# Kernel optimization log

Hardware: AMD Instinct MI355X
Metric: run time of the kernel (lower is better)

## Reference

```python
import jax, jax.numpy as jnp
import numpy as np
import math

B, S, D, H = 2, 2048, 2048, 16
HD = D // H  # head_dim = 128


def _rope_tables(seq_len, head_dim, theta=10000.0):
    inv = 1.0 / (theta ** (np.arange(0, head_dim, 2, dtype=np.float32) / head_dim))
    t = np.arange(seq_len, dtype=np.float32)
    freqs = np.outer(t, inv)  # [S, HD/2]
    return jnp.asarray(np.cos(freqs)), jnp.asarray(np.sin(freqs))


def setup_inputs() -> dict:
    key = jax.random.key(0)
    ks = jax.random.split(key, 6)
    std = 1.0 / math.sqrt(D)
    x = jax.random.normal(ks[0], (B, S, D), dtype=jnp.float32)
    wq_w = jax.random.normal(ks[1], (D, D), dtype=jnp.float32) * std
    wk_w = jax.random.normal(ks[2], (D, D), dtype=jnp.float32) * std
    wv_w = jax.random.normal(ks[3], (D, D), dtype=jnp.float32) * std
    wo_w = jax.random.normal(ks[4], (D, D), dtype=jnp.float32) * std
    zb = jnp.zeros((D,), dtype=jnp.float32)
    fc, fs = _rope_tables(S, HD)
    return {"x": x, "wq_w": wq_w, "wq_b": zb, "wk_w": wk_w, "wk_b": zb,
            "wv_w": wv_w, "wv_b": zb, "wo_w": wo_w, "wo_b": zb,
            "freqs_cos": fc, "freqs_sin": fs}


def _apply_rope(q, k, cos, sin):
    # q, k: [B, S, H, HD]; cos/sin: [S, HD/2] -> broadcast [1, S, 1, HD/2]
    cos = cos[None, :, None, :]
    sin = sin[None, :, None, :]

    def rot(t):
        tr, ti = t[..., 0::2], t[..., 1::2]
        orr = tr * cos - ti * sin
        oi = tr * sin + ti * cos
        return jnp.stack([orr, oi], axis=-1).reshape(t.shape)

    return rot(q), rot(k)


def reference(x, wq_w, wq_b, wk_w, wk_b, wv_w, wv_b, wo_w, wo_b, freqs_cos, freqs_sin):
    b, s, d = x.shape
    q = (x @ wq_w.T + wq_b).reshape(b, s, H, HD)
    k = (x @ wk_w.T + wk_b).reshape(b, s, H, HD)
    v = (x @ wv_w.T + wv_b).reshape(b, s, H, HD)
    q, k = _apply_rope(q, k, freqs_cos[:s], freqs_sin[:s])
    q = q.transpose(0, 2, 1, 3)  # [B,H,S,HD]
    k = k.transpose(0, 2, 1, 3)
    v = v.transpose(0, 2, 1, 3)
    scale = math.sqrt(HD)
    scores = jnp.einsum('bhqd,bhkd->bhqk', q, k) / scale
    causal = jnp.tril(jnp.ones((s, s), dtype=bool))
    scores = jnp.where(causal[None, None], scores, jnp.float32(-jnp.inf))
    attn = jax.nn.softmax(scores, axis=-1)
    out = jnp.einsum('bhqk,bhkd->bhqd', attn, v)
    out = out.transpose(0, 2, 1, 3).reshape(b, s, d)
    out = out @ wo_w.T + wo_b
    return out, k, v
```

## Files before the change

### kernel.cpp

```cpp
#include <hip/hip_runtime.h>

#define B_  2
#define S_  2048
#define D_  2048
#define H_  16
#define HD_ 128

#define QSCALE 0.1275174319003887f

typedef __attribute__((ext_vector_type(4))) float  f32x4;
typedef __attribute__((ext_vector_type(8))) short  short8;
typedef __attribute__((ext_vector_type(8))) __bf16 bf16x8;
typedef __attribute__((ext_vector_type(4))) float  floatv4;
typedef __attribute__((ext_vector_type(4))) unsigned short ushortv4;

__device__ inline unsigned short f2bf(float f) {
  unsigned int u = __builtin_bit_cast(unsigned int, f);
  u += 0x7fffu + ((u >> 16) & 1u);
  return (unsigned short)(u >> 16);
}

__device__ inline void gld16(void* lds, const void* g) {
  __builtin_amdgcn_global_load_lds(
      (const __attribute__((address_space(1))) unsigned int*)g,
      (__attribute__((address_space(3))) unsigned int*)lds, 16, 0, 0);
}

__device__ inline bf16x8 lds_frag(const unsigned short* p) {
  return __builtin_bit_cast(bf16x8, *(const short8*)p);
}

__global__ void cvt_all(const float* __restrict__ x,
                        const float* __restrict__ w0, const float* __restrict__ w1,
                        const float* __restrict__ w2, const float* __restrict__ w3,
                        unsigned short* __restrict__ xb,
                        unsigned short* __restrict__ wb0, unsigned short* __restrict__ wb1,
                        unsigned short* __restrict__ wb2, unsigned short* __restrict__ wb3) {
  int i = blockIdx.x * 256 + threadIdx.x;
  const float* s; unsigned short* d; int off;
  if (i < 2097152) { s = x; d = xb; off = i; }
  else {
    int j = i - 2097152;
    int r = j >> 20; off = j & 1048575;
    s = (r == 0) ? w0 : (r == 1) ? w1 : (r == 2) ? w2 : w3;
    d = (r == 0) ? wb0 : (r == 1) ? wb1 : (r == 2) ? wb2 : wb3;
  }
  floatv4 v = ((const floatv4*)s)[off];
  ushortv4 o;
  o.x = f2bf(v.x); o.y = f2bf(v.y); o.z = f2bf(v.z); o.w = f2bf(v.w);
  ((ushortv4*)d)[off] = o;
}

__global__ __launch_bounds__(256, 2)
void gemm_nt(const unsigned short* __restrict__ A,
             const unsigned short* __restrict__ W,
             const float* __restrict__ bias,
             float* __restrict__ C, int M, int N, int K) {
  __shared__ __attribute__((aligned(16))) unsigned short As[128 * 32];
  __shared__ __attribute__((aligned(16))) unsigned short Bs[128 * 32];
  const int t = threadIdx.x;
  const int w = t >> 6, lane = t & 63;
  const int quad = lane >> 4, l16 = lane & 15;
  const int m0 = blockIdx.y * 128, n0 = blockIdx.x * 128;
  const int wm = (w >> 1) * 64, wn = (w & 1) * 64;
  f32x4 acc[4][4] = {};

  for (int k0 = 0; k0 < K; k0 += 32) {
    __syncthreads();
#pragma unroll
    for (int j = 0; j < 2; ++j) {
      int o = (t + 256 * j) * 16;
      int row = o >> 6, cb = o & 63;
      gld16((char*)As + w * 1024 + j * 4096,
            (const char*)(A + (size_t)(m0 + row) * K + k0) + cb);
      gld16((char*)Bs + w * 1024 + j * 4096,
            (const char*)(W + (size_t)(n0 + row) * K + k0) + cb);
    }
    __syncthreads();
    bf16x8 af[4], bfr[4];
#pragma unroll
    for (int i = 0; i < 4; ++i)
      af[i] = lds_frag(As + (wm + i * 16 + l16) * 32 + quad * 8);
#pragma unroll
    for (int j = 0; j < 4; ++j)
      bfr[j] = lds_frag(Bs + (wn + j * 16 + l16) * 32 + quad * 8);
#pragma unroll
    for (int i = 0; i < 4; ++i)
#pragma unroll
      for (int j = 0; j < 4; ++j)
        acc[i][j] = __builtin_amdgcn_mfma_f32_16x16x32_bf16(af[i], bfr[j], acc[i][j], 0, 0, 0);
  }

#pragma unroll
  for (int j = 0; j < 4; ++j) {
    int col = n0 + wn + j * 16 + l16;
    float bv = bias[col];
#pragma unroll
    for (int i = 0; i < 4; ++i)
#pragma unroll
      for (int r = 0; r < 4; ++r) {
        int row = m0 + wm + i * 16 + quad * 4 + r;
        C[(size_t)row * N + col] = acc[i][j][r] + bv;
      }
  }
}

__global__ void rope_kernel(const float* __restrict__ Qbuf,
                            const float* __restrict__ Kbuf,
                            const float* __restrict__ fc,
                            const float* __restrict__ fs,
                            unsigned short* __restrict__ Qa,
                            unsigned short* __restrict__ Ka,
                            float* __restrict__ k_out) {
  int idx = blockIdx.x * 256 + threadIdx.x;
  int i = idx & 63;
  int h = (idx >> 6) & (H_ - 1);
  int s = (idx >> 10) & (S_ - 1);
  int b = idx >> 21;
  size_t src = ((size_t)(b * S_ + s)) * D_ + h * HD_ + 2 * i;
  float2 q = *(const float2*)(Qbuf + src);
  float2 k = *(const float2*)(Kbuf + src);
  float c = fc[s * 64 + i], sn = fs[s * 64 + i];
  float qor = q.x * c - q.y * sn, qoi = q.x * sn + q.y * c;
  float kor = k.x * c - k.y * sn, koi = k.x * sn + k.y * c;
  size_t dst = ((size_t)((b * H_ + h) * S_ + s)) * HD_ + 2 * i;
  *(unsigned int*)(Qa + dst) = (unsigned int)f2bf(qor * QSCALE) | ((unsigned int)f2bf(qoi * QSCALE) << 16);
  *(unsigned int*)(Ka + dst) = (unsigned int)f2bf(kor) | ((unsigned int)f2bf(koi) << 16);
  *(float2*)(k_out + dst) = make_float2(kor, koi);
}

__global__ void vtrans_kernel(const float* __restrict__ Vbuf,
                              float* __restrict__ v_out,
                              unsigned short* __restrict__ Vt) {
  __shared__ float tile[64][33];
  int t = threadIdx.x;
  int s0 = blockIdx.x * 64, d0 = blockIdx.y * 32, bh = blockIdx.z;
  int b = bh >> 4, h = bh & 15;
#pragma unroll
  for (int rr = 0; rr < 8; ++rr) {
    int sl = rr * 8 + (t >> 5), dl = t & 31;
    float v = Vbuf[((size_t)(b * S_ + s0 + sl)) * D_ + h * HD_ + d0 + dl];
    tile[sl][dl] = v;
    v_out[((size_t)(bh * S_ + s0 + sl)) * HD_ + d0 + dl] = v;
  }
  __syncthreads();
#pragma unroll
  for (int rr = 0; rr < 8; ++rr) {
    int dl = rr * 4 + (t >> 6), sl = t & 63;
    Vt[((size_t)(bh * HD_ + d0 + dl)) * S_ + s0 + sl] = f2bf(tile[sl][dl]);
  }
}

__global__ __launch_bounds__(256, 2)
void attn_kernel(const unsigned short* __restrict__ Qa,
                 const unsigned short* __restrict__ Ka,
                 const unsigned short* __restrict__ Vt,
                 unsigned short* __restrict__ Oa) {
  __shared__ __attribute__((aligned(16))) unsigned short Ks[2][64 * 128];
  __shared__ __attribute__((aligned(16))) unsigned short Vs[128 * 64];
  __shared__ __attribute__((aligned(16))) unsigned short Ps[4][32 * 64];
  const int t = threadIdx.x, w = t >> 6, lane = t & 63;
  const int quad = lane >> 4, l16 = lane & 15;
  const int bh = blockIdx.y, b = bh >> 4, h = bh & 15;
  const unsigned short* Qp = Qa + (size_t)bh * S_ * HD_;
  const unsigned short* Kp = Ka + (size_t)bh * S_ * HD_;
  const unsigned short* Vp = Vt + (size_t)bh * HD_ * S_;
  const float NEGINF = -__builtin_inff();

  for (int part = 0; part < 2; ++part) {
    const int qt = part ? (15 - (int)blockIdx.x) : (int)blockIdx.x;
    const int q0 = qt * 128;
    const int ntmax = 2 * qt + 1;

    __syncthreads();

#pragma unroll
    for (int j = 0; j < 4; ++j) {
      int o = (t + 256 * j) * 16;
      int row = o >> 8, cb = o & 255;
      gld16((char*)Ks[0] + w * 1024 + j * 4096, (const char*)(Kp + (size_t)row * HD_) + cb);
    }
    bf16x8 qf[2][4];
#pragma unroll
    for (int mi = 0; mi < 2; ++mi)
#pragma unroll
      for (int kk = 0; kk < 4; ++kk)
        qf[mi][kk] = *(const bf16x8*)(Qp + (size_t)(q0 + w * 32 + mi * 16 + l16) * HD_ + kk * 32 + quad * 8);

    float m_i[2][4], l_i[2][4];
#pragma unroll
    for (int mi = 0; mi < 2; ++mi)
#pragma unroll
      for (int r = 0; r < 4; ++r) { m_i[mi][r] = NEGINF; l_i[mi][r] = 0.f; }
    f32x4 oacc[2][8] = {};
    int c = 0;

    for (int nt = 0; nt <= ntmax; ++nt) {
      __syncthreads();

#pragma unroll
      for (int j = 0; j < 4; ++j) {
        int o = (t + 256 * j) * 16;
        int vrow = o >> 7, vcb = o & 127;
        gld16((char*)Vs + w * 1024 + j * 4096,
              (const char*)(Vp + (size_t)vrow * S_ + nt * 64) + vcb);
      }

      f32x4 sacc[2][4] = {};
      const unsigned short* Kc = Ks[c];
#pragma unroll
      for (int j = 0; j < 4; ++j)
#pragma unroll
        for (int kk = 0; kk < 4; ++kk) {
          bf16x8 kf = lds_frag(Kc + (j * 16 + l16) * 128 + kk * 32 + quad * 8);
          sacc[0][j] = __builtin_amdgcn_mfma_f32_16x16x32_bf16(qf[0][kk], kf, sacc[0][j], 0, 0, 0);
          sacc[1][j] = __builtin_amdgcn_mfma_f32_16x16x32_bf16(qf[1][kk], kf, sacc[1][j], 0, 0, 0);
        }

      const bool dotail = (nt >= 2 * qt);
      float rowmax[2][4], alpha[2][4], rowsum[2][4];
#pragma unroll
      for (int mi = 0; mi < 2; ++mi)
#pragma unroll
        for (int r = 0; r < 4; ++r) rowmax[mi][r] = NEGINF;
#pragma unroll
      for (int mi = 0; mi < 2; ++mi)
#pragma unroll
        for (int j = 0; j < 4; ++j) {
          int scol = nt * 64 + j * 16 + l16;
#pragma unroll
          for (int r = 0; r < 4; ++r) {
            float v = sacc[mi][j][r];
            if (dotail && scol > q0 + w * 32 + mi * 16 + quad * 4 + r) v = NEGINF;
            sacc[mi][j][r] = v;
            rowmax[mi][r] = fmaxf(rowmax[mi][r], v);
          }
        }
#pragma unroll
      for (int off = 1; off < 16; off <<= 1)
#pragma unroll
        for (int mi = 0; mi < 2; ++mi)
#pragma unroll
          for (int r = 0; r < 4; ++r)
            rowmax[mi][r] = fmaxf(rowmax[mi][r], __shfl_xor(rowmax[mi][r], off));
#pragma unroll
      for (int mi = 0; mi < 2; ++mi)
#pragma unroll
        for (int r = 0; r < 4; ++r) {
          float mnew = fmaxf(m_i[mi][r], rowmax[mi][r]);
          alpha[mi][r] = __builtin_amdgcn_exp2f(m_i[mi][r] - mnew);
          m_i[mi][r] = mnew;
          rowsum[mi][r] = 0.f;
        }
#pragma unroll
      for (int mi = 0; mi < 2; ++mi)
#pragma unroll
        for (int j = 0; j < 4; ++j)
#pragma unroll
          for (int r = 0; r < 4; ++r) {
            float e = __builtin_amdgcn_exp2f(sacc[mi][j][r] - m_i[mi][r]);
            sacc[mi][j][r] = e;
            rowsum[mi][r] += e;
          }
#pragma unroll
      for (int off = 1; off < 16; off <<= 1)
#pragma unroll
        for (int mi = 0; mi < 2; ++mi)
#pragma unroll
          for (int r = 0; r < 4; ++r)
            rowsum[mi][r] += __shfl_xor(rowsum[mi][r], off);
#pragma unroll
      for (int mi = 0; mi < 2; ++mi)
#pragma unroll
        for (int r = 0; r < 4; ++r) l_i[mi][r] = l_i[mi][r] * alpha[mi][r] + rowsum[mi][r];
#pragma unroll
      for (int mi = 0; mi < 2; ++mi)
#pragma unroll
        for (int f = 0; f < 8; ++f)
#pragma unroll
          for (int r = 0; r < 4; ++r) oacc[mi][f][r] *= alpha[mi][r];

      __syncthreads();

      if (nt < ntmax) {
#pragma unroll
        for (int j = 0; j < 4; ++j) {
          int o = (t + 256 * j) * 16;
          int row = o >> 8, cb = o & 255;
          gld16((char*)Ks[c ^ 1] + w * 1024 + j * 4096,
                (const char*)(Kp + (size_t)((nt + 1) * 64 + row) * HD_) + cb);
        }
      }

      unsigned short* Pw = &Ps[w][0];
#pragma unroll
      for (int mi = 0; mi < 2; ++mi)
#pragma unroll
        for (int j = 0; j < 4; ++j)
#pragma unroll
          for (int r = 0; r < 4; ++r)
            Pw[(mi * 16 + quad * 4 + r) * 64 + j * 16 + l16] = f2bf(sacc[mi][j][r]);
      asm volatile("s_waitcnt lgkmcnt(0)" ::: "memory");

#pragma unroll
      for (int s2 = 0; s2 < 2; ++s2) {
        bf16x8 pf0 = lds_frag(Pw + (l16) * 64 + s2 * 32 + quad * 8);
        bf16x8 pf1 = lds_frag(Pw + (16 + l16) * 64 + s2 * 32 + quad * 8);
#pragma unroll
        for (int f = 0; f < 8; ++f) {
          bf16x8 vf = lds_frag(Vs + (f * 16 + l16) * 64 + s2 * 32 + quad * 8);
          oacc[0][f] = __builtin_amdgcn_mfma_f32_16x16x32_bf16(pf0, vf, oacc[0][f], 0, 0, 0);
          oacc[1][f] = __builtin_amdgcn_mfma_f32_16x16x32_bf16(pf1, vf, oacc[1][f], 0, 0, 0);
        }
      }
      c ^= 1;
    }

#pragma unroll
    for (int mi = 0; mi < 2; ++mi) {
      float invl[4];
#pragma unroll
      for (int r = 0; r < 4; ++r) invl[r] = 1.f / l_i[mi][r];
#pragma unroll
      for (int f = 0; f < 8; ++f)
#pragma unroll
        for (int r = 0; r < 4; ++r) {
          int srow = q0 + w * 32 + mi * 16 + quad * 4 + r;
          int d = f * 16 + l16;
          Oa[((size_t)(b * S_ + srow)) * D_ + h * HD_ + d] = f2bf(oacc[mi][f][r] * invl[r]);
        }
    }
  }
}

extern "C" void kernel_launch(void* const* d_in, const int* in_sizes, int n_in,
                              void* d_out, int out_size, void* d_ws, size_t ws_size,
                              hipStream_t stream) {
  const float* x    = (const float*)d_in[0];
  const float* wq_w = (const float*)d_in[1];
  const float* wq_b = (const float*)d_in[2];
  const float* wk_w = (const float*)d_in[3];
  const float* wk_b = (const float*)d_in[4];
  const float* wv_w = (const float*)d_in[5];
  const float* wv_b = (const float*)d_in[6];
  const float* wo_w = (const float*)d_in[7];
  const float* wo_b = (const float*)d_in[8];
  const float* fc   = (const float*)d_in[9];
  const float* fs   = (const float*)d_in[10];

  float* out = (float*)d_out;
  const size_t BSD = (size_t)B_ * S_ * D_;
  float* k_out = out + BSD;
  float* v_out = out + 2 * BSD;

  char* ws = (char*)d_ws;
  unsigned short* xb   = (unsigned short*)(ws);
  unsigned short* wqb  = (unsigned short*)(ws + 16777216);
  unsigned short* wkb  = (unsigned short*)(ws + 25165824);
  unsigned short* wvb  = (unsigned short*)(ws + 33554432);
  unsigned short* wob  = (unsigned short*)(ws + 41943040);
  float*          Vbuf = (float*)(ws + 50331648);
  unsigned short* Qat  = (unsigned short*)(ws + 83886080);
  unsigned short* Kat  = (unsigned short*)(ws + 100663296);
  unsigned short* Vt   = (unsigned short*)(ws + 117440512);
  unsigned short* Ab   = (unsigned short*)(ws + 134217728);

  float* Qbuf = out;
  float* Kbuf = v_out;

  cvt_all<<<24576, 256, 0, stream>>>(x, wq_w, wk_w, wv_w, wo_w, xb, wqb, wkb, wvb, wob);

  dim3 gg(16, 32);
  gemm_nt<<<gg, 256, 0, stream>>>(xb, wqb, wq_b, Qbuf, 4096, 2048, 2048);
  gemm_nt<<<gg, 256, 0, stream>>>(xb, wkb, wk_b, Kbuf, 4096, 2048, 2048);
  gemm_nt<<<gg, 256, 0, stream>>>(xb, wvb, wv_b, Vbuf, 4096, 2048, 2048);

  rope_kernel<<<16384, 256, 0, stream>>>(Qbuf, Kbuf, fc, fs, Qat, Kat, k_out);
  vtrans_kernel<<<dim3(32, 4, 32), 256, 0, stream>>>(Vbuf, v_out, Vt);
  attn_kernel<<<dim3(8, 32), 256, 0, stream>>>(Qat, Kat, Vt, Ab);
  gemm_nt<<<gg, 256, 0, stream>>>(Ab, wob, wo_b, out, 4096, 2048, 2048);
}
```

Measured before the change: 544.4 us.

## Fuse QKV projections into one GEMM and retile attention with swizzled LDS

Replaces the three separate Q/K/V projection GEMM launches with one kernel over a 48x32 grid. It relies on the contiguous wq/wk/wv bf16 weight buffers to treat them as one 6144-row matrix and routes each output column block to the right buffer and bias. The attention kernel now uses 64-row query tiles with 16 rows per wave, on a 1D grid of 512 blocks with a head-interleaved block mapping. K, V and P tiles in LDS get an XOR swizzle to avoid bank conflicts. Smaller tiles mean more blocks and less per-wave register pressure, but also less reuse of each loaded K/V tile across query rows.

```diff
diff --git a/kernel.cpp b/kernel.cpp
--- a/kernel.cpp
+++ b/kernel.cpp
@@ -27,6 +27,9 @@
 }
 
 __device__ inline bf16x8 lds_frag(const unsigned short* p) {
+  return __builtin_bit_cast(bf16x8, *(const short8*)p);
+}
+__device__ inline bf16x8 lds_frag_b(const void* p) {
   return __builtin_bit_cast(bf16x8, *(const short8*)p);
 }
 
@@ -101,6 +104,65 @@
       for (int r = 0; r < 4; ++r) {
         int row = m0 + wm + i * 16 + quad * 4 + r;
         C[(size_t)row * N + col] = acc[i][j][r] + bv;
+      }
+  }
+}
+
+__global__ __launch_bounds__(256, 2)
+void gemm_qkv(const unsigned short* __restrict__ A,
+              const unsigned short* __restrict__ W,
+              const float* __restrict__ b0, const float* __restrict__ b1, const float* __restrict__ b2,
+              float* __restrict__ C0, float* __restrict__ C1, float* __restrict__ C2,
+              int K) {
+  __shared__ __attribute__((aligned(16))) unsigned short As[128 * 32];
+  __shared__ __attribute__((aligned(16))) unsigned short Bs[128 * 32];
+  const int t = threadIdx.x;
+  const int w = t >> 6, lane = t & 63;
+  const int quad = lane >> 4, l16 = lane & 15;
+  const int m0 = blockIdx.y * 128, n0 = blockIdx.x * 128;
+  const int wm = (w >> 1) * 64, wn = (w & 1) * 64;
+  f32x4 acc[4][4] = {};
+
+  for (int k0 = 0; k0 < K; k0 += 32) {
+    __syncthreads();
+#pragma unroll
+    for (int j = 0; j < 2; ++j) {
+      int o = (t + 256 * j) * 16;
+      int row = o >> 6, cb = o & 63;
+      gld16((char*)As + w * 1024 + j * 4096,
+            (const char*)(A + (size_t)(m0 + row) * K + k0) + cb);
+      gld16((char*)Bs + w * 1024 + j * 4096,
+            (const char*)(W + (size_t)(n0 + row) * K + k0) + cb);
+    }
+    __syncthreads();
+    bf16x8 af[4], bfr[4];
+#pragma unroll
+    for (int i = 0; i < 4; ++i)
+      af[i] = lds_frag(As + (wm + i * 16 + l16) * 32 + quad * 8);
+#pragma unroll
+    for (int j = 0; j < 4; ++j)
+      bfr[j] = lds_frag(Bs + (wn + j * 16 + l16) * 32 + quad * 8);
+#pragma unroll
+    for (int i = 0; i < 4; ++i)
+#pragma unroll
+      for (int j = 0; j < 4; ++j)
+        acc[i][j] = __builtin_amdgcn_mfma_f32_16x16x32_bf16(af[i], bfr[j], acc[i][j], 0, 0, 0);
+  }
+
+#pragma unroll
+  for (int j = 0; j < 4; ++j) {
+    int col = n0 + wn + j * 16 + l16;
+    int sel = col >> 11;
+    const float* bp = (sel == 0) ? b0 : (sel == 1) ? b1 : b2;
+    float* Cd      = (sel == 0) ? C0 : (sel == 1) ? C1 : C2;
+    int cc = col & 2047;
+    float bv = bp[cc];
+#pragma unroll
+    for (int i = 0; i < 4; ++i)
+#pragma unroll
+      for (int r = 0; r < 4; ++r) {
+        int row = m0 + wm + i * 16 + quad * 4 + r;
+        Cd[(size_t)row * 2048 + cc] = acc[i][j][r] + bv;
       }
   }
 }
@@ -158,41 +220,40 @@
                  unsigned short* __restrict__ Oa) {
   __shared__ __attribute__((aligned(16))) unsigned short Ks[2][64 * 128];
   __shared__ __attribute__((aligned(16))) unsigned short Vs[128 * 64];
-  __shared__ __attribute__((aligned(16))) unsigned short Ps[4][32 * 64];
+  __shared__ __attribute__((aligned(16))) unsigned short Ps[4][16 * 64];
   const int t = threadIdx.x, w = t >> 6, lane = t & 63;
   const int quad = lane >> 4, l16 = lane & 15;
-  const int bh = blockIdx.y, b = bh >> 4, h = bh & 15;
+  const int bid = blockIdx.x;
+  const int bh = (bid & 7) + 8 * (bid >> 7);
+  const int p  = (bid >> 3) & 15;
+  const int b = bh >> 4, h = bh & 15;
   const unsigned short* Qp = Qa + (size_t)bh * S_ * HD_;
   const unsigned short* Kp = Ka + (size_t)bh * S_ * HD_;
   const unsigned short* Vp = Vt + (size_t)bh * HD_ * S_;
   const float NEGINF = -__builtin_inff();
 
   for (int part = 0; part < 2; ++part) {
-    const int qt = part ? (15 - (int)blockIdx.x) : (int)blockIdx.x;
-    const int q0 = qt * 128;
-    const int ntmax = 2 * qt + 1;
+    const int qs = part ? (31 - p) : p;
+    const int q0 = qs * 64;
+    const int ntmax = qs;
 
     __syncthreads();
 
 #pragma unroll
     for (int j = 0; j < 4; ++j) {
       int o = (t + 256 * j) * 16;
-      int row = o >> 8, cb = o & 255;
+      int row = o >> 8, cb = (o & 255) ^ ((row & 7) << 4);
       gld16((char*)Ks[0] + w * 1024 + j * 4096, (const char*)(Kp + (size_t)row * HD_) + cb);
     }
-    bf16x8 qf[2][4];
-#pragma unroll
-    for (int mi = 0; mi < 2; ++mi)
-#pragma unroll
-      for (int kk = 0; kk < 4; ++kk)
-        qf[mi][kk] = *(const bf16x8*)(Qp + (size_t)(q0 + w * 32 + mi * 16 + l16) * HD_ + kk * 32 + quad * 8);
-
-    float m_i[2][4], l_i[2][4];
-#pragma unroll
-    for (int mi = 0; mi < 2; ++mi)
-#pragma unroll
-      for (int r = 0; r < 4; ++r) { m_i[mi][r] = NEGINF; l_i[mi][r] = 0.f; }
-    f32x4 oacc[2][8] = {};
+    bf16x8 qf[4];
+#pragma unroll
+    for (int kk = 0; kk < 4; ++kk)
+      qf[kk] = *(const bf16x8*)(Qp + (size_t)(q0 + w * 16 + l16) * HD_ + kk * 32 + quad * 8);
+
+    float m_i[4], l_i[4];
+#pragma unroll
+    for (int r = 0; r < 4; ++r) { m_i[r] = NEGINF; l_i[r] = 0.f; }
+    f32x4 oacc[8] = {};
     int c = 0;
 
     for (int nt = 0; nt <= ntmax; ++nt) {
@@ -201,84 +262,71 @@
 #pragma unroll
       for (int j = 0; j < 4; ++j) {
         int o = (t + 256 * j) * 16;
-        int vrow = o >> 7, vcb = o & 127;
+        int vrow = o >> 7, vcb = (o & 127) ^ ((vrow & 7) << 4);
         gld16((char*)Vs + w * 1024 + j * 4096,
               (const char*)(Vp + (size_t)vrow * S_ + nt * 64) + vcb);
       }
 
-      f32x4 sacc[2][4] = {};
-      const unsigned short* Kc = Ks[c];
+      f32x4 sacc[4] = {};
+      const char* Kc = (const char*)Ks[c];
+#pragma unroll
+      for (int j = 0; j < 4; ++j) {
+        int krow = j * 16 + l16;
+        const char* kbase = Kc + krow * 256;
+        int ksw = (krow & 7) << 4;
+#pragma unroll
+        for (int kk = 0; kk < 4; ++kk) {
+          bf16x8 kf = lds_frag_b(kbase + ((kk * 64 + quad * 16) ^ ksw));
+          sacc[j] = __builtin_amdgcn_mfma_f32_16x16x32_bf16(qf[kk], kf, sacc[j], 0, 0, 0);
+        }
+      }
+
+      const bool dotail = (nt == ntmax);
+      float rowmax[4], alpha[4], rowsum[4];
+#pragma unroll
+      for (int r = 0; r < 4; ++r) rowmax[r] = NEGINF;
+#pragma unroll
+      for (int j = 0; j < 4; ++j) {
+        int scol = nt * 64 + j * 16 + l16;
+#pragma unroll
+        for (int r = 0; r < 4; ++r) {
+          float v = sacc[j][r];
+          if (dotail && scol > q0 + w * 16 + quad * 4 + r) v = NEGINF;
+          sacc[j][r] = v;
+          rowmax[r] = fmaxf(rowmax[r], v);
+        }
+      }
+#pragma unroll
+      for (int off = 1; off < 16; off <<= 1)
+#pragma unroll
+        for (int r = 0; r < 4; ++r)
+          rowmax[r] = fmaxf(rowmax[r], __shfl_xor(rowmax[r], off));
+#pragma unroll
+      for (int r = 0; r < 4; ++r) {
+        float mnew = fmaxf(m_i[r], rowmax[r]);
+        alpha[r] = __builtin_amdgcn_exp2f(m_i[r] - mnew);
+        m_i[r] = mnew;
+        rowsum[r] = 0.f;
+      }
 #pragma unroll
       for (int j = 0; j < 4; ++j)
 #pragma unroll
-        for (int kk = 0; kk < 4; ++kk) {
-          bf16x8 kf = lds_frag(Kc + (j * 16 + l16) * 128 + kk * 32 + quad * 8);
-          sacc[0][j] = __builtin_amdgcn_mfma_f32_16x16x32_bf16(qf[0][kk], kf, sacc[0][j], 0, 0, 0);
-          sacc[1][j] = __builtin_amdgcn_mfma_f32_16x16x32_bf16(qf[1][kk], kf, sacc[1][j], 0, 0, 0);
-        }
-
-      const bool dotail = (nt >= 2 * qt);
-      float rowmax[2][4], alpha[2][4], rowsum[2][4];
-#pragma unroll
-      for (int mi = 0; mi < 2; ++mi)
-#pragma unroll
-        for (int r = 0; r < 4; ++r) rowmax[mi][r] = NEGINF;
-#pragma unroll
-      for (int mi = 0; mi < 2; ++mi)
-#pragma unroll
-        for (int j = 0; j < 4; ++j) {
-          int scol = nt * 64 + j * 16 + l16;
-#pragma unroll
-          for (int r = 0; r < 4; ++r) {
-            float v = sacc[mi][j][r];
-            if (dotail && scol > q0 + w * 32 + mi * 16 + quad * 4 + r) v = NEGINF;
-            sacc[mi][j][r] = v;
-            rowmax[mi][r] = fmaxf(rowmax[mi][r], v);
-          }
+        for (int r = 0; r < 4; ++r) {
+          float e = __builtin_amdgcn_exp2f(sacc[j][r] - m_i[r]);
+          sacc[j][r] = e;
+          rowsum[r] += e;
         }
 #pragma unroll
       for (int off = 1; off < 16; off <<= 1)
 #pragma unroll
-        for (int mi = 0; mi < 2; ++mi)
-#pragma unroll
-          for (int r = 0; r < 4; ++r)
-            rowmax[mi][r] = fmaxf(rowmax[mi][r], __shfl_xor(rowmax[mi][r], off));
-#pragma unroll
-      for (int mi = 0; mi < 2; ++mi)
-#pragma unroll
-        for (int r = 0; r < 4; ++r) {
-          float mnew = fmaxf(m_i[mi][r], rowmax[mi][r]);
-          alpha[mi][r] = __builtin_amdgcn_exp2f(m_i[mi][r] - mnew);
-          m_i[mi][r] = mnew;
-          rowsum[mi][r] = 0.f;
-        }
-#pragma unroll
-      for (int mi = 0; mi < 2; ++mi)
-#pragma unroll
-        for (int j = 0; j < 4; ++j)
-#pragma unroll
-          for (int r = 0; r < 4; ++r) {
-            float e = __builtin_amdgcn_exp2f(sacc[mi][j][r] - m_i[mi][r]);
-            sacc[mi][j][r] = e;
-            rowsum[mi][r] += e;
-          }
-#pragma unroll
-      for (int off = 1; off < 16; off <<= 1)
-#pragma unroll
-        for (int mi = 0; mi < 2; ++mi)
-#pragma unroll
-          for (int r = 0; r < 4; ++r)
-            rowsum[mi][r] += __shfl_xor(rowsum[mi][r], off);
-#pragma unroll
-      for (int mi = 0; mi < 2; ++mi)
-#pragma unroll
-        for (int r = 0; r < 4; ++r) l_i[mi][r] = l_i[mi][r] * alpha[mi][r] + rowsum[mi][r];
-#pragma unroll
-      for (int mi = 0; mi < 2; ++mi)
-#pragma unroll
-        for (int f = 0; f < 8; ++f)
-#pragma unroll
-          for (int r = 0; r < 4; ++r) oacc[mi][f][r] *= alpha[mi][r];
+        for (int r = 0; r < 4; ++r)
+          rowsum[r] += __shfl_xor(rowsum[r], off);
+#pragma unroll
+      for (int r = 0; r < 4; ++r) l_i[r] = l_i[r] * alpha[r] + rowsum[r];
+#pragma unroll
+      for (int f = 0; f < 8; ++f)
+#pragma unroll
+        for (int r = 0; r < 4; ++r) oacc[f][r] *= alpha[r];
 
       __syncthreads();
 
@@ -286,50 +334,48 @@
 #pragma unroll
         for (int j = 0; j < 4; ++j) {
           int o = (t + 256 * j) * 16;
-          int row = o >> 8, cb = o & 255;
+          int row = o >> 8, cb = (o & 255) ^ ((row & 7) << 4);
           gld16((char*)Ks[c ^ 1] + w * 1024 + j * 4096,
                 (const char*)(Kp + (size_t)((nt + 1) * 64 + row) * HD_) + cb);
         }
       }
 
-      unsigned short* Pw = &Ps[w][0];
-#pragma unroll
-      for (int mi = 0; mi < 2; ++mi)
-#pragma unroll
-        for (int j = 0; j < 4; ++j)
-#pragma unroll
-          for (int r = 0; r < 4; ++r)
-            Pw[(mi * 16 + quad * 4 + r) * 64 + j * 16 + l16] = f2bf(sacc[mi][j][r]);
+      char* Pw = (char*)&Ps[w][0];
+#pragma unroll
+      for (int j = 0; j < 4; ++j)
+#pragma unroll
+        for (int r = 0; r < 4; ++r) {
+          int prow = quad * 4 + r;
+          *(unsigned short*)(Pw + prow * 128 + ((2 * (j * 16 + l16)) ^ ((prow & 7) << 4))) = f2bf(sacc[j][r]);
+        }
       asm volatile("s_waitcnt lgkmcnt(0)" ::: "memory");
 
+      const char* Vb = (const char*)Vs;
+      int psw = (l16 & 7) << 4;
 #pragma unroll
       for (int s2 = 0; s2 < 2; ++s2) {
-        bf16x8 pf0 = lds_frag(Pw + (l16) * 64 + s2 * 32 + quad * 8);
-        bf16x8 pf1 = lds_frag(Pw + (16 + l16) * 64 + s2 * 32 + quad * 8);
+        bf16x8 pf = lds_frag_b(Pw + l16 * 128 + ((s2 * 64 + quad * 16) ^ psw));
 #pragma unroll
         for (int f = 0; f < 8; ++f) {
-          bf16x8 vf = lds_frag(Vs + (f * 16 + l16) * 64 + s2 * 32 + quad * 8);
-          oacc[0][f] = __builtin_amdgcn_mfma_f32_16x16x32_bf16(pf0, vf, oacc[0][f], 0, 0, 0);
-          oacc[1][f] = __builtin_amdgcn_mfma_f32_16x16x32_bf16(pf1, vf, oacc[1][f], 0, 0, 0);
+          int vrow = f * 16 + l16;
+          bf16x8 vf = lds_frag_b(Vb + vrow * 128 + ((s2 * 64 + quad * 16) ^ ((vrow & 7) << 4)));
+          oacc[f] = __builtin_amdgcn_mfma_f32_16x16x32_bf16(pf, vf, oacc[f], 0, 0, 0);
         }
       }
       c ^= 1;
     }
 
-#pragma unroll
-    for (int mi = 0; mi < 2; ++mi) {
-      float invl[4];
-#pragma unroll
-      for (int r = 0; r < 4; ++r) invl[r] = 1.f / l_i[mi][r];
-#pragma unroll
-      for (int f = 0; f < 8; ++f)
-#pragma unroll
-        for (int r = 0; r < 4; ++r) {
-          int srow = q0 + w * 32 + mi * 16 + quad * 4 + r;
-          int d = f * 16 + l16;
-          Oa[((size_t)(b * S_ + srow)) * D_ + h * HD_ + d] = f2bf(oacc[mi][f][r] * invl[r]);
-        }
-    }
+    float invl[4];
+#pragma unroll
+    for (int r = 0; r < 4; ++r) invl[r] = 1.f / l_i[r];
+#pragma unroll
+    for (int f = 0; f < 8; ++f)
+#pragma unroll
+      for (int r = 0; r < 4; ++r) {
+        int srow = q0 + w * 16 + quad * 4 + r;
+        int d = f * 16 + l16;
+        Oa[((size_t)(b * S_ + srow)) * D_ + h * HD_ + d] = f2bf(oacc[f][r] * invl[r]);
+      }
   }
 }
 
@@ -370,13 +416,11 @@
 
   cvt_all<<<24576, 256, 0, stream>>>(x, wq_w, wk_w, wv_w, wo_w, xb, wqb, wkb, wvb, wob);
 
-  dim3 gg(16, 32);
-  gemm_nt<<<gg, 256, 0, stream>>>(xb, wqb, wq_b, Qbuf, 4096, 2048, 2048);
-  gemm_nt<<<gg, 256, 0, stream>>>(xb, wkb, wk_b, Kbuf, 4096, 2048, 2048);
-  gemm_nt<<<gg, 256, 0, stream>>>(xb, wvb, wv_b, Vbuf, 4096, 2048, 2048);
+  gemm_qkv<<<dim3(48, 32), 256, 0, stream>>>(xb, wqb, wq_b, wk_b, wv_b,
+                                             Qbuf, Kbuf, Vbuf, 2048);
 
   rope_kernel<<<16384, 256, 0, stream>>>(Qbuf, Kbuf, fc, fs, Qat, Kat, k_out);
   vtrans_kernel<<<dim3(32, 4, 32), 256, 0, stream>>>(Vbuf, v_out, Vt);
-  attn_kernel<<<dim3(8, 32), 256, 0, stream>>>(Qat, Kat, Vt, Ab);
-  gemm_nt<<<gg, 256, 0, stream>>>(Ab, wob, wo_b, out, 4096, 2048, 2048);
-}
+  attn_kernel<<<512, 256, 0, stream>>>(Qat, Kat, Vt, Ab);
+  gemm_nt<<<dim3(16, 32), 256, 0, stream>>>(Ab, wob, wo_b, out, 4096, 2048, 2048);
+}
```

Result: faster. 476.3 us (-12.5%).
